# Optimization experiments

Hardware: AMD Instinct MI355X
Metric: run time of the kernel (lower is better)

Reference implementation:

```python
import jax, jax.numpy as jnp
import numpy as np

B, D, H, M = 32, 1024, 1024, 2048
HEBBIAN_LR = 0.05
SCALE = 0.5
TEMP = 1.5
SPARSITY = 0.1
EPS_LN = 1e-6


def _l2_normalize(v, axis=-1):
    # matches tf.nn.l2_normalize: x * rsqrt(max(sum(x^2), 1e-12))
    sq = jnp.sum(v * v, axis=axis, keepdims=True)
    return v * jax.lax.rsqrt(jnp.maximum(sq, 1e-12))


def _layer_norm(v, gamma, beta):
    mu = jnp.mean(v, axis=-1, keepdims=True)
    var = jnp.mean((v - mu) ** 2, axis=-1, keepdims=True)
    return (v - mu) * jax.lax.rsqrt(var + EPS_LN) * gamma + beta


def setup_inputs() -> dict:
    key = jax.random.key(0)
    ks = jax.random.split(key, 8)
    s = 0.02
    return {
        "x": jax.random.normal(ks[0], (B, D), jnp.float32),
        "prev_h": jax.random.normal(ks[1], (B, H), jnp.float32) * 0.01,
        "hebbian_trace": jax.random.normal(ks[2], (M, H), jnp.float32) * 0.01,
        "memory_bank": jax.random.normal(ks[3], (M, H), jnp.float32) * s,
        "W_enc": jax.random.normal(ks[4], (D, H), jnp.float32) * s,
        "b_enc": jnp.zeros((H,), jnp.float32),
        "gamma1": jnp.ones((H,), jnp.float32),
        "beta1": jnp.zeros((H,), jnp.float32),
        "W_int": jax.random.normal(ks[5], (3 * H, 3 * H), jnp.float32) * s,
        "b_int": jnp.zeros((3 * H,), jnp.float32),
        "W_out": jax.random.normal(ks[6], (3 * H, H), jnp.float32) * s,
        "b_out": jnp.zeros((H,), jnp.float32),
        "gamma2": jnp.ones((H,), jnp.float32),
        "beta2": jnp.zeros((H,), jnp.float32),
    }


def reference(x, prev_h, hebbian_trace, memory_bank,
              W_enc, b_enc, gamma1, beta1,
              W_int, b_int, W_out, b_out, gamma2, beta2):
    # input encoder + LN
    z_t = jax.nn.relu(x @ W_enc + b_enc)          # [B,H]
    z_t = _layer_norm(z_t, gamma1, beta1)
    # effective memory = bank + scale * hebbian trace
    eff_mem = memory_bank + SCALE * hebbian_trace  # [M,H]
    # cosine-similarity attention over memory slots
    z_n = _l2_normalize(z_t)
    m_n = _l2_normalize(eff_mem)
    sim = z_n @ m_n.T                               # [B,M]
    sparsity_temp = TEMP / (1.0 + SPARSITY * 10.0)  # = 0.75
    attn = jax.nn.softmax(sim / sparsity_temp, axis=-1)
    m_t = attn @ eff_mem                            # [B,H]
    # integrate and output
    combined = jnp.concatenate([z_t, m_t, prev_h], axis=-1)  # [B,3H]
    hidden = jax.nn.relu(combined @ W_int + b_int)
    h_t = jax.nn.relu(hidden @ W_out + b_out)
    h_t = _layer_norm(h_t, gamma2, beta2)
    # Hebbian trace update: batch-mean outer product attn^T z / B
    mean_update = (attn.T @ z_t) / jnp.asarray(attn.shape[0], z_t.dtype)  # [M,H]
    noise = jax.random.normal(jax.random.key(42), mean_update.shape, mean_update.dtype) * 0.001
    decay = 1.0 - HEBBIAN_LR
    new_trace = hebbian_trace * decay + HEBBIAN_LR * (mean_update + noise)
    new_trace = jnp.clip(new_trace, -0.1, 0.1)
    return h_t, new_trace
```

## Files before the change

### kernel.cpp

```cpp
#include <hip/hip_runtime.h>

typedef unsigned short u16;
typedef unsigned int u32;

#define NB 32
#define NH 1024
#define NM 2048
#define NH3 3072

#define O_Z     0
#define O_RZ    32768
#define O_MT    32800
#define O_HID   65568
#define O_BIG   163872
#define O_ATTN  (O_BIG)
#define O_ATTNP (O_BIG + 65536)
#define O_SQP   (O_BIG + 1114112)
#define O_MTP2  (O_BIG + 65536)
#define O_LMS   (O_BIG + 1146944)

static __device__ __forceinline__ float bf2f(u16 u) {
  union { u32 i; float f; } v; v.i = ((u32)u) << 16; return v.f;
}
static __device__ __forceinline__ u16 f2bf(float f) {
  union { float f; u32 u; } v; v.f = f;
  u32 r = v.u + 0x7FFFu + ((v.u >> 16) & 1u);
  return (u16)(r >> 16);
}
template <bool F32>
static __device__ __forceinline__ float ldT(const void* p, int i) {
  if (F32) return ((const float*)p)[i];
  return bf2f(((const u16*)p)[i]);
}
template <bool F32>
static __device__ __forceinline__ void ld8(const void* p, long i, float o[8]) {
  if (F32) {
    const float4* q = (const float4*)p;
    float4 a = q[i >> 2], b = q[(i >> 2) + 1];
    o[0] = a.x; o[1] = a.y; o[2] = a.z; o[3] = a.w;
    o[4] = b.x; o[5] = b.y; o[6] = b.z; o[7] = b.w;
  } else {
    uint4 u = ((const uint4*)p)[i >> 3];
    o[0] = bf2f((u16)u.x); o[1] = bf2f((u16)(u.x >> 16));
    o[2] = bf2f((u16)u.y); o[3] = bf2f((u16)(u.y >> 16));
    o[4] = bf2f((u16)u.z); o[5] = bf2f((u16)(u.z >> 16));
    o[6] = bf2f((u16)u.w); o[7] = bf2f((u16)(u.w >> 16));
  }
}
template <bool F32>
static __device__ __forceinline__ void st8(void* p, long i, const float o[8]) {
  if (F32) {
    float4* q = (float4*)p;
    float4 a = {o[0], o[1], o[2], o[3]}, b = {o[4], o[5], o[6], o[7]};
    q[i >> 2] = a; q[(i >> 2) + 1] = b;
  } else {
    uint4 u;
    u.x = (u32)f2bf(o[0]) | ((u32)f2bf(o[1]) << 16);
    u.y = (u32)f2bf(o[2]) | ((u32)f2bf(o[3]) << 16);
    u.z = (u32)f2bf(o[4]) | ((u32)f2bf(o[5]) << 16);
    u.w = (u32)f2bf(o[6]) | ((u32)f2bf(o[7]) << 16);
    ((uint4*)p)[i >> 3] = u;
  }
}
template <bool F32>
static __device__ __forceinline__ void stT(void* p, int i, float v) {
  if (F32) ((float*)p)[i] = v;
  else ((u16*)p)[i] = f2bf(v);
}

template <bool F32>
static __device__ __forceinline__ void gemm_core(
    const void* W, int ldw, int k0, int K0, int j0, const float* cs,
    float* dst, int ldd, int l, int w) {
  const int cg = l >> 4, cl = l & 15;
  float acc[8][8];
#pragma unroll
  for (int r = 0; r < 8; ++r)
#pragma unroll
    for (int c = 0; c < 8; ++c) acc[r][c] = 0.f;
#pragma unroll 2
  for (int kk = cg; kk < K0; kk += 4) {
    float wv[8];
    ld8<F32>(W, (long)(k0 + kk) * ldw + j0 + cl * 8, wv);
    const float4* zr = (const float4*)(cs + kk * 36 + w * 8);
    float4 a0 = zr[0], a1 = zr[1];
    float a[8] = {a0.x, a0.y, a0.z, a0.w, a1.x, a1.y, a1.z, a1.w};
#pragma unroll
    for (int r = 0; r < 8; ++r)
#pragma unroll
      for (int c = 0; c < 8; ++c) acc[r][c] += a[r] * wv[c];
  }
#pragma unroll
  for (int r = 0; r < 8; ++r)
#pragma unroll
    for (int c = 0; c < 8; ++c) {
      acc[r][c] += __shfl_xor(acc[r][c], 16);
      acc[r][c] += __shfl_xor(acc[r][c], 32);
    }
#pragma unroll
  for (int r = 0; r < 8; ++r) {
    if ((r >> 1) == cg) {
      float* d = dst + (long)(w * 8 + r) * ldd + j0 + cl * 8;
      float4 v0 = {acc[r][0], acc[r][1], acc[r][2], acc[r][3]};
      float4 v1 = {acc[r][4], acc[r][5], acc[r][6], acc[r][7]};
      ((float4*)d)[0] = v0;
      ((float4*)d)[1] = v1;
    }
  }
}

template <bool F32>
static __device__ void phases(
    int phase, const void* x, const void* prev_h, const void* trace,
    const void* bank, const void* W_enc, const void* b_enc, const void* g1,
    const void* be1, const void* W_int, const void* b_int, const void* W_out,
    const void* b_out, const void* g2, const void* be2, void* outv, float* ws,
    float* sm) {
  const int t = threadIdx.x;
  const int l = t & 63, w = t >> 6;
  const int bx = blockIdx.x;

  if (phase == 1) {
    int j0 = (bx & 7) * 128, ks = bx >> 3, k0 = ks * 64;
    float* cs = sm;
    for (int i = 0; i < 8; ++i) {
      int idx = t + 256 * i; int kk = idx >> 5, bb = idx & 31;
      cs[kk * 36 + bb] = ldT<F32>(x, bb * NH + k0 + kk);
    }
    __syncthreads();
    gemm_core<F32>(W_enc, NH, k0, 64, j0, cs, ws + O_BIG + ks * 32768, NH, l, w);
  } else if (phase == 2) {
    float* red = sm;
    int b = bx, h = t * 4;
    float vv[4];
    vv[0] = ldT<F32>(b_enc, h);     vv[1] = ldT<F32>(b_enc, h + 1);
    vv[2] = ldT<F32>(b_enc, h + 2); vv[3] = ldT<F32>(b_enc, h + 3);
    for (int p = 0; p < 16; ++p) {
      const float4 pv = *(const float4*)&ws[O_BIG + p * 32768 + b * NH + h];
      vv[0] += pv.x; vv[1] += pv.y; vv[2] += pv.z; vv[3] += pv.w;
    }
    float s = 0.f, sq = 0.f;
#pragma unroll
    for (int i = 0; i < 4; ++i) {
      vv[i] = fmaxf(vv[i], 0.f); s += vv[i]; sq += vv[i] * vv[i];
    }
    red[t] = s; __syncthreads();
    for (int d = 128; d > 0; d >>= 1) { if (t < d) red[t] += red[t + d]; __syncthreads(); }
    s = red[0]; __syncthreads();
    red[t] = sq; __syncthreads();
    for (int d = 128; d > 0; d >>= 1) { if (t < d) red[t] += red[t + d]; __syncthreads(); }
    sq = red[0]; __syncthreads();
    float mu = s * (1.f / NH);
    float inv = rsqrtf(sq * (1.f / NH) - mu * mu + 1e-6f);
    float y[4]; float ss = 0.f;
#pragma unroll
    for (int i = 0; i < 4; ++i) {
      y[i] = (vv[i] - mu) * inv * ldT<F32>(g1, h + i) + ldT<F32>(be1, h + i);
      ss += y[i] * y[i];
    }
    float4 y4 = {y[0], y[1], y[2], y[3]};
    *(float4*)&ws[O_Z + b * NH + h] = y4;
    red[t] = ss; __syncthreads();
    for (int d = 128; d > 0; d >>= 1) { if (t < d) red[t] += red[t + d]; __syncthreads(); }
    if (t == 0) ws[O_RZ + b] = rsqrtf(fmaxf(red[0], 1e-12f));
  } else if (phase == 3) {
    int m0 = (bx & 31) * 64, ks = bx >> 5, k0 = ks * 256;
    float* zs = sm;
    for (int i = 0; i < 32; ++i) {
      int idx = t + 256 * i; int kk = idx >> 5, bb = idx & 31;
      zs[idx] = ws[O_Z + bb * NH + k0 + kk];
    }
    __syncthreads();
    int m = m0 + l;
    float acc[32];
#pragma unroll
    for (int i = 0; i < 32; ++i) acc[i] = 0.f;
    float sq = 0.f;
    long rowb = (long)m * NH + k0 + w * 64;
    const float4* zq = (const float4*)(zs + w * 64 * 32);
#pragma unroll 2
    for (int it = 0; it < 8; ++it) {
      float eb[8], et[8];
      ld8<F32>(bank, rowb + it * 8, eb);
      ld8<F32>(trace, rowb + it * 8, et);
#pragma unroll
      for (int kk = 0; kk < 8; ++kk) {
        float e = eb[kk] + 0.5f * et[kk];
        sq += e * e;
        const float4* z4 = zq + (it * 8 + kk) * 8;
#pragma unroll
        for (int bq = 0; bq < 8; ++bq) {
          float4 zv = z4[bq];
          acc[bq * 4 + 0] += e * zv.x; acc[bq * 4 + 1] += e * zv.y;
          acc[bq * 4 + 2] += e * zv.z; acc[bq * 4 + 3] += e * zv.w;
        }
      }
    }
    int p = ks * 4 + w;
#pragma unroll
    for (int bb = 0; bb < 32; ++bb)
      ws[O_ATTNP + p * 65536 + bb * NM + m] = acc[bb];
    ws[O_SQP + p * NM + m] = sq;
  } else if (phase == 4) {
    float* red = sm;
    int b = bx >> 3, mc = bx & 7;
    int m = mc * 256 + t;
    float dot = 0.f, sq = 0.f;
    for (int p = 0; p < 16; ++p) {
      dot += ws[O_ATTNP + p * 65536 + b * NM + m];
      sq  += ws[O_SQP + p * NM + m];
    }
    float rzb = ws[O_RZ + b] * (4.0f / 3.0f);
    float lg = dot * rzb * rsqrtf(fmaxf(sq, 1e-12f));
    ws[O_ATTN + b * NM + m] = lg;
    red[t] = lg; __syncthreads();
    for (int d = 128; d > 0; d >>= 1) { if (t < d) red[t] = fmaxf(red[t], red[t + d]); __syncthreads(); }
    float mx = red[0]; __syncthreads();
    red[t] = __expf(lg - mx); __syncthreads();
    for (int d = 128; d > 0; d >>= 1) { if (t < d) red[t] += red[t + d]; __syncthreads(); }
    if (t == 0) {
      ws[O_LMS + (b * 8 + mc) * 2] = mx;
      ws[O_LMS + (b * 8 + mc) * 2 + 1] = red[0];
    }
  } else if (phase == 5) {
    int j0 = (bx & 7) * 128, ms = bx >> 3, m0 = ms * 64;
    float* cs = sm;
    float* msh = sm + 2304;
    if (t < 32) {
      float M = -1e30f; float lm[8];
#pragma unroll
      for (int i = 0; i < 8; ++i) { lm[i] = ws[O_LMS + (t * 8 + i) * 2]; M = fmaxf(M, lm[i]); }
      float S = 0.f;
#pragma unroll
      for (int i = 0; i < 8; ++i) S += ws[O_LMS + (t * 8 + i) * 2 + 1] * __expf(lm[i] - M);
      msh[2 * t] = M; msh[2 * t + 1] = 1.f / S;
    }
    __syncthreads();
    for (int i = 0; i < 8; ++i) {
      int idx = t + 256 * i; int kk = idx >> 5, bb = idx & 31;
      float lg = ws[O_ATTN + bb * NM + m0 + kk];
      cs[kk * 36 + bb] = __expf(lg - msh[2 * bb]) * msh[2 * bb + 1];
    }
    __syncthreads();
    const int cg = l >> 4, cl = l & 15;
    float acc[8][8];
#pragma unroll
    for (int r = 0; r < 8; ++r)
#pragma unroll
      for (int c = 0; c < 8; ++c) acc[r][c] = 0.f;
#pragma unroll 2
    for (int kk = cg; kk < 64; kk += 4) {
      float eb[8], et[8];
      long src = (long)(m0 + kk) * NH + j0 + cl * 8;
      ld8<F32>(bank, src, eb);
      ld8<F32>(trace, src, et);
      const float4* ar4 = (const float4*)(cs + kk * 36 + w * 8);
      float4 a0 = ar4[0], a1 = ar4[1];
      float a[8] = {a0.x, a0.y, a0.z, a0.w, a1.x, a1.y, a1.z, a1.w};
      float e[8];
#pragma unroll
      for (int c = 0; c < 8; ++c) e[c] = eb[c] + 0.5f * et[c];
#pragma unroll
      for (int r = 0; r < 8; ++r)
#pragma unroll
        for (int c = 0; c < 8; ++c) acc[r][c] += a[r] * e[c];
    }
#pragma unroll
    for (int r = 0; r < 8; ++r)
#pragma unroll
      for (int c = 0; c < 8; ++c) {
        acc[r][c] += __shfl_xor(acc[r][c], 16);
        acc[r][c] += __shfl_xor(acc[r][c], 32);
      }
#pragma unroll
    for (int r = 0; r < 8; ++r) {
      if ((r >> 1) == cg) {
        float* d = ws + O_MTP2 + ms * 32768 + (long)(w * 8 + r) * NH + j0 + cl * 8;
        float4 v0 = {acc[r][0], acc[r][1], acc[r][2], acc[r][3]};
        float4 v1 = {acc[r][4], acc[r][5], acc[r][6], acc[r][7]};
        ((float4*)d)[0] = v0;
        ((float4*)d)[1] = v1;
      }
    }
  } else if (phase == 11) {
    int idx = bx * 256 + t;
    float v = 0.f;
    for (int p = 0; p < 32; ++p) v += ws[O_MTP2 + p * 32768 + idx];
    ws[O_MT + idx] = v;
  } else if (phase == 6) {
    int m0 = (bx >> 3) * 32, h0 = (bx & 7) * 128;
    float* as = sm;
    float* zs = sm + 1024;
    float* msh = sm + 5120;
    if (t < 32) {
      float M = -1e30f; float lm[8];
#pragma unroll
      for (int i = 0; i < 8; ++i) { lm[i] = ws[O_LMS + (t * 8 + i) * 2]; M = fmaxf(M, lm[i]); }
      float S = 0.f;
#pragma unroll
      for (int i = 0; i < 8; ++i) S += ws[O_LMS + (t * 8 + i) * 2 + 1] * __expf(lm[i] - M);
      msh[2 * t] = M; msh[2 * t + 1] = 1.f / S;
    }
    __syncthreads();
    for (int i = 0; i < 4; ++i) {
      int idx = t + 256 * i; int bb = idx >> 5, mm = idx & 31;
      as[idx] = __expf(ws[O_ATTN + bb * NM + m0 + mm] - msh[2 * bb]) * msh[2 * bb + 1];
    }
    for (int i = 0; i < 16; ++i) {
      int idx = t + 256 * i; int bb = idx >> 7, hh = idx & 127;
      zs[idx] = ws[O_Z + bb * NH + h0 + hh];
    }
    __syncthreads();
    const int cg = l >> 4, cl = l & 15;
    const int mA = m0 + cl * 2;
    const int h = h0 + w * 32 + cg * 8;
    float acc0[8], acc1[8];
#pragma unroll
    for (int c = 0; c < 8; ++c) { acc0[c] = 0.f; acc1[c] = 0.f; }
    for (int bb = 0; bb < 32; ++bb) {
      float2 av = *(const float2*)&as[bb * 32 + cl * 2];
      const float4* zr = (const float4*)&zs[bb * 128 + w * 32 + cg * 8];
      float4 z0 = zr[0], z1 = zr[1];
      acc0[0] += av.x * z0.x; acc0[1] += av.x * z0.y;
      acc0[2] += av.x * z0.z; acc0[3] += av.x * z0.w;
      acc0[4] += av.x * z1.x; acc0[5] += av.x * z1.y;
      acc0[6] += av.x * z1.z; acc0[7] += av.x * z1.w;
      acc1[0] += av.y * z0.x; acc1[1] += av.y * z0.y;
      acc1[2] += av.y * z0.z; acc1[3] += av.y * z0.w;
      acc1[4] += av.y * z1.x; acc1[5] += av.y * z1.y;
      acc1[6] += av.y * z1.z; acc1[7] += av.y * z1.w;
    }
    {
      int m = mA;
      float tv[8], o[8];
      ld8<F32>(trace, (long)m * NH + h, tv);
#pragma unroll
      for (int c = 0; c < 8; ++c) {
        float val = tv[c] * 0.95f + 0.0015625f * acc0[c];
        o[c] = fminf(fmaxf(val, -0.1f), 0.1f);
      }
      st8<F32>(outv, (long)NB * NH + (long)m * NH + h, o);
    }
    {
      int m = mA + 1;
      float tv[8], o[8];
      ld8<F32>(trace, (long)m * NH + h, tv);
#pragma unroll
      for (int c = 0; c < 8; ++c) {
        float val = tv[c] * 0.95f + 0.0015625f * acc1[c];
        o[c] = fminf(fmaxf(val, -0.1f), 0.1f);
      }
      st8<F32>(outv, (long)NB * NH + (long)m * NH + h, o);
    }
  } else if (phase == 7) {
    int jc = bx % 24, ks = bx / 24;
    int j0 = jc * 128, k0 = ks * 256;
    float* cs = sm;
    if (ks < 4) {
      for (int i = 0; i < 32; ++i) {
        int idx = t + 256 * i; int kk = idx >> 5, bb = idx & 31;
        cs[kk * 36 + bb] = ws[O_Z + bb * NH + k0 + kk];
      }
    } else if (ks < 8) {
      for (int i = 0; i < 32; ++i) {
        int idx = t + 256 * i; int kk = idx >> 5, bb = idx & 31;
        cs[kk * 36 + bb] = ws[O_MT + bb * NH + (k0 - 1024) + kk];
      }
    } else {
      for (int i = 0; i < 32; ++i) {
        int idx = t + 256 * i; int kk = idx >> 5, bb = idx & 31;
        cs[kk * 36 + bb] = ldT<F32>(prev_h, bb * NH + (k0 - 2048) + kk);
      }
    }
    __syncthreads();
    gemm_core<F32>(W_int, NH3, k0, 256, j0, cs, ws + O_BIG + ks * 98304, NH3, l, w);
  } else if (phase == 8) {
    int idx4 = bx * 256 + t;
    int j = (idx4 % 768) * 4;
    float v0 = ldT<F32>(b_int, j),     v1 = ldT<F32>(b_int, j + 1);
    float v2 = ldT<F32>(b_int, j + 2), v3 = ldT<F32>(b_int, j + 3);
    const float4* pb = (const float4*)(ws + O_BIG);
    for (int p = 0; p < 12; ++p) {
      float4 pv = pb[p * 24576 + idx4];
      v0 += pv.x; v1 += pv.y; v2 += pv.z; v3 += pv.w;
    }
    float4 o = {fmaxf(v0, 0.f), fmaxf(v1, 0.f), fmaxf(v2, 0.f), fmaxf(v3, 0.f)};
    ((float4*)(ws + O_HID))[idx4] = o;
  } else if (phase == 9) {
    int j0 = (bx & 7) * 128, ks = bx >> 3, k0 = ks * 128;
    float* cs = sm;
    for (int i = 0; i < 16; ++i) {
      int idx = t + 256 * i; int kk = idx >> 5, bb = idx & 31;
      cs[kk * 36 + bb] = ws[O_HID + bb * NH3 + k0 + kk];
    }
    __syncthreads();
    gemm_core<F32>(W_out, NH, k0, 128, j0, cs, ws + O_BIG + ks * 32768, NH, l, w);
  } else if (phase == 10) {
    float* red = sm;
    int b = bx, h = t * 4;
    float vv[4];
    vv[0] = ldT<F32>(b_out, h);     vv[1] = ldT<F32>(b_out, h + 1);
    vv[2] = ldT<F32>(b_out, h + 2); vv[3] = ldT<F32>(b_out, h + 3);
    for (int p = 0; p < 24; ++p) {
      const float4 pv = *(const float4*)&ws[O_BIG + p * 32768 + b * NH + h];
      vv[0] += pv.x; vv[1] += pv.y; vv[2] += pv.z; vv[3] += pv.w;
    }
    float s = 0.f, sq = 0.f;
#pragma unroll
    for (int i = 0; i < 4; ++i) {
      vv[i] = fmaxf(vv[i], 0.f); s += vv[i]; sq += vv[i] * vv[i];
    }
    red[t] = s; __syncthreads();
    for (int d = 128; d > 0; d >>= 1) { if (t < d) red[t] += red[t + d]; __syncthreads(); }
    s = red[0]; __syncthreads();
    red[t] = sq; __syncthreads();
    for (int d = 128; d > 0; d >>= 1) { if (t < d) red[t] += red[t + d]; __syncthreads(); }
    sq = red[0];
    float mu = s * (1.f / NH);
    float inv = rsqrtf(sq * (1.f / NH) - mu * mu + 1e-6f);
#pragma unroll
    for (int i = 0; i < 4; ++i) {
      float y = (vv[i] - mu) * inv * ldT<F32>(g2, h + i) + ldT<F32>(be2, h + i);
      stT<F32>(outv, b * NH + h + i, y);
    }
  }
}

__global__ __launch_bounds__(256, 2) void EngramCell_82935818485852_kernel(
    int phase,
    const void* x, const void* prev_h, const void* trace, const void* bank,
    const void* W_enc, const void* b_enc, const void* g1, const void* be1,
    const void* W_int, const void* b_int, const void* W_out, const void* b_out,
    const void* g2, const void* be2,
    void* outv, float* ws) {
  __shared__ float sm[9216];
  const bool f32m = (((const u32*)g1)[0] == 0x3F800000u);
  if (f32m)
    phases<true>(phase, x, prev_h, trace, bank, W_enc, b_enc, g1, be1,
                 W_int, b_int, W_out, b_out, g2, be2, outv, ws, sm);
  else
    phases<false>(phase, x, prev_h, trace, bank, W_enc, b_enc, g1, be1,
                  W_int, b_int, W_out, b_out, g2, be2, outv, ws, sm);
}

extern "C" void kernel_launch(void* const* d_in, const int* in_sizes, int n_in,
                              void* d_out, int out_size, void* d_ws, size_t ws_size,
                              hipStream_t stream) {
  (void)in_sizes; (void)n_in; (void)out_size; (void)ws_size;
  const void* x      = d_in[0];
  const void* prev_h = d_in[1];
  const void* trace  = d_in[2];
  const void* bank   = d_in[3];
  const void* W_enc  = d_in[4];
  const void* b_enc  = d_in[5];
  const void* g1     = d_in[6];
  const void* be1    = d_in[7];
  const void* W_int  = d_in[8];
  const void* b_int  = d_in[9];
  const void* W_out  = d_in[10];
  const void* b_out  = d_in[11];
  const void* g2     = d_in[12];
  const void* be2    = d_in[13];
  float* ws = (float*)d_ws;

  const int order[11] = {1, 2, 3, 4, 5, 11, 6, 7, 8, 9, 10};
  const int grids[12] = {0, 128, 32, 128, 256, 256, 512, 288, 384, 192, 32, 128};
  for (int i = 0; i < 11; ++i) {
    int ph = order[i];
    EngramCell_82935818485852_kernel<<<grids[ph], 256, 0, stream>>>(
        ph, x, prev_h, trace, bank, W_enc, b_enc, g1, be1,
        W_int, b_int, W_out, b_out, g2, be2, d_out, ws);
  }
}
```

Before: 226.7 us.

## Collapse eleven phase launches into six fused phases without split-K partial buffers

Reorganizes the multi-launch pipeline into six phases. The encoder GEMM is fused with its layer norm per batch row. The similarity GEMM now reduces over K inside a block and computes per-chunk softmax statistics. The m_t computation and the trace update share one launch, and the two dense GEMMs reduce over K in-block, so the split-K partial buffers and their separate reduction kernels are gone. This removes global round trips and launch overhead. The cost is far fewer blocks for the big GEMMs (96 and 32), which risks underusing the GPU's compute units and lengthening the serial K loops.

```diff
diff --git a/kernel.cpp b/kernel.cpp
--- a/kernel.cpp
+++ b/kernel.cpp
@@ -14,10 +14,7 @@
 #define O_HID   65568
 #define O_BIG   163872
 #define O_ATTN  (O_BIG)
-#define O_ATTNP (O_BIG + 65536)
-#define O_SQP   (O_BIG + 1114112)
-#define O_MTP2  (O_BIG + 65536)
-#define O_LMS   (O_BIG + 1146944)
+#define O_LMS2  (O_BIG + 65536)
 
 static __device__ __forceinline__ float bf2f(u16 u) {
   union { u32 i; float f; } v; v.i = ((u32)u) << 16; return v.f;
@@ -31,6 +28,12 @@
 static __device__ __forceinline__ float ldT(const void* p, int i) {
   if (F32) return ((const float*)p)[i];
   return bf2f(((const u16*)p)[i]);
+}
+template <bool F32>
+static __device__ __forceinline__ float2 ld2T(const void* p, long i) {
+  if (F32) return ((const float2*)p)[i >> 1];
+  u32 u = ((const u32*)p)[i >> 1];
+  float2 r; r.x = bf2f((u16)u); r.y = bf2f((u16)(u >> 16)); return r;
 }
 template <bool F32>
 static __device__ __forceinline__ void ld8(const void* p, long i, float o[8]) {
@@ -69,48 +72,7 @@
 }
 
 template <bool F32>
-static __device__ __forceinline__ void gemm_core(
-    const void* W, int ldw, int k0, int K0, int j0, const float* cs,
-    float* dst, int ldd, int l, int w) {
-  const int cg = l >> 4, cl = l & 15;
-  float acc[8][8];
-#pragma unroll
-  for (int r = 0; r < 8; ++r)
-#pragma unroll
-    for (int c = 0; c < 8; ++c) acc[r][c] = 0.f;
-#pragma unroll 2
-  for (int kk = cg; kk < K0; kk += 4) {
-    float wv[8];
-    ld8<F32>(W, (long)(k0 + kk) * ldw + j0 + cl * 8, wv);
-    const float4* zr = (const float4*)(cs + kk * 36 + w * 8);
-    float4 a0 = zr[0], a1 = zr[1];
-    float a[8] = {a0.x, a0.y, a0.z, a0.w, a1.x, a1.y, a1.z, a1.w};
-#pragma unroll
-    for (int r = 0; r < 8; ++r)
-#pragma unroll
-      for (int c = 0; c < 8; ++c) acc[r][c] += a[r] * wv[c];
-  }
-#pragma unroll
-  for (int r = 0; r < 8; ++r)
-#pragma unroll
-    for (int c = 0; c < 8; ++c) {
-      acc[r][c] += __shfl_xor(acc[r][c], 16);
-      acc[r][c] += __shfl_xor(acc[r][c], 32);
-    }
-#pragma unroll
-  for (int r = 0; r < 8; ++r) {
-    if ((r >> 1) == cg) {
-      float* d = dst + (long)(w * 8 + r) * ldd + j0 + cl * 8;
-      float4 v0 = {acc[r][0], acc[r][1], acc[r][2], acc[r][3]};
-      float4 v1 = {acc[r][4], acc[r][5], acc[r][6], acc[r][7]};
-      ((float4*)d)[0] = v0;
-      ((float4*)d)[1] = v1;
-    }
-  }
-}
-
-template <bool F32>
-static __device__ void phases(
+static __device__ void run_phase(
     int phase, const void* x, const void* prev_h, const void* trace,
     const void* bank, const void* W_enc, const void* b_enc, const void* g1,
     const void* be1, const void* W_int, const void* b_int, const void* W_out,
@@ -121,73 +83,91 @@
   const int bx = blockIdx.x;
 
   if (phase == 1) {
-    int j0 = (bx & 7) * 128, ks = bx >> 3, k0 = ks * 64;
-    float* cs = sm;
-    for (int i = 0; i < 8; ++i) {
-      int idx = t + 256 * i; int kk = idx >> 5, bb = idx & 31;
-      cs[kk * 36 + bb] = ldT<F32>(x, bb * NH + k0 + kk);
-    }
-    __syncthreads();
-    gemm_core<F32>(W_enc, NH, k0, 64, j0, cs, ws + O_BIG + ks * 32768, NH, l, w);
-  } else if (phase == 2) {
-    float* red = sm;
-    int b = bx, h = t * 4;
-    float vv[4];
-    vv[0] = ldT<F32>(b_enc, h);     vv[1] = ldT<F32>(b_enc, h + 1);
-    vv[2] = ldT<F32>(b_enc, h + 2); vv[3] = ldT<F32>(b_enc, h + 3);
-    for (int p = 0; p < 16; ++p) {
-      const float4 pv = *(const float4*)&ws[O_BIG + p * 32768 + b * NH + h];
-      vv[0] += pv.x; vv[1] += pv.y; vv[2] += pv.z; vv[3] += pv.w;
-    }
-    float s = 0.f, sq = 0.f;
-#pragma unroll
-    for (int i = 0; i < 4; ++i) {
-      vv[i] = fmaxf(vv[i], 0.f); s += vv[i]; sq += vv[i] * vv[i];
+    int b = bx;
+    {
+      float2 v = ld2T<F32>(x, (long)b * NH + 2 * t);
+      sm[2 * t] = v.x; sm[2 * t + 1] = v.y;
+    }
+    __syncthreads();
+    const int tj = t & 127, ts = t >> 7;
+    const int j0 = tj * 8;
+    float acc[8];
+#pragma unroll
+    for (int i = 0; i < 8; ++i) acc[i] = 0.f;
+#pragma unroll 2
+    for (int kk = 0; kk < 256; ++kk) {
+      int k = ts * 256 + kk;
+      float wv[8];
+      ld8<F32>(W_enc, (long)k * NH + j0, wv);
+      float xv = sm[k];
+#pragma unroll
+      for (int i = 0; i < 8; ++i) acc[i] += xv * wv[i];
+    }
+    float* rd = sm + 1024;
+    {
+      float4 a = {acc[0], acc[1], acc[2], acc[3]};
+      float4 c = {acc[4], acc[5], acc[6], acc[7]};
+      *(float4*)&rd[(ts * 128 + tj) * 8] = a;
+      *(float4*)&rd[(ts * 128 + tj) * 8 + 4] = c;
+    }
+    __syncthreads();
+    float* red = sm + 5120;
+    float vv[2]; float s = 0.f, sq = 0.f;
+#pragma unroll
+    for (int jj = 0; jj < 2; ++jj) {
+      int j = t * 2 + jj;
+      float v = ldT<F32>(b_enc, j);
+#pragma unroll
+      for (int q = 0; q < 4; ++q) v += rd[(q * 128 + (j >> 3)) * 8 + (j & 7)];
+      v = fmaxf(v, 0.f);
+      vv[jj] = v; s += v; sq += v * v;
     }
     red[t] = s; __syncthreads();
-    for (int d = 128; d > 0; d >>= 1) { if (t < d) red[t] += red[t + d]; __syncthreads(); }
+    for (int d = 256; d > 0; d >>= 1) { if (t < d) red[t] += red[t + d]; __syncthreads(); }
     s = red[0]; __syncthreads();
     red[t] = sq; __syncthreads();
-    for (int d = 128; d > 0; d >>= 1) { if (t < d) red[t] += red[t + d]; __syncthreads(); }
+    for (int d = 256; d > 0; d >>= 1) { if (t < d) red[t] += red[t + d]; __syncthreads(); }
     sq = red[0]; __syncthreads();
     float mu = s * (1.f / NH);
     float inv = rsqrtf(sq * (1.f / NH) - mu * mu + 1e-6f);
-    float y[4]; float ss = 0.f;
-#pragma unroll
-    for (int i = 0; i < 4; ++i) {
-      y[i] = (vv[i] - mu) * inv * ldT<F32>(g1, h + i) + ldT<F32>(be1, h + i);
-      ss += y[i] * y[i];
-    }
-    float4 y4 = {y[0], y[1], y[2], y[3]};
-    *(float4*)&ws[O_Z + b * NH + h] = y4;
+    float y[2]; float ss = 0.f;
+#pragma unroll
+    for (int jj = 0; jj < 2; ++jj) {
+      int j = t * 2 + jj;
+      y[jj] = (vv[jj] - mu) * inv * ldT<F32>(g1, j) + ldT<F32>(be1, j);
+      ss += y[jj] * y[jj];
+    }
+    float2 y2 = {y[0], y[1]};
+    *(float2*)&ws[O_Z + b * NH + t * 2] = y2;
     red[t] = ss; __syncthreads();
-    for (int d = 128; d > 0; d >>= 1) { if (t < d) red[t] += red[t + d]; __syncthreads(); }
+    for (int d = 256; d > 0; d >>= 1) { if (t < d) red[t] += red[t + d]; __syncthreads(); }
     if (t == 0) ws[O_RZ + b] = rsqrtf(fmaxf(red[0], 1e-12f));
-  } else if (phase == 3) {
-    int m0 = (bx & 31) * 64, ks = bx >> 5, k0 = ks * 256;
+
+  } else if (phase == 2) {
+    const int m0 = bx * 32;
+    const int m = m0 + (l & 31);
+    const int s = w * 2 + (l >> 5);
     float* zs = sm;
-    for (int i = 0; i < 32; ++i) {
-      int idx = t + 256 * i; int kk = idx >> 5, bb = idx & 31;
-      zs[idx] = ws[O_Z + bb * NH + k0 + kk];
-    }
-    __syncthreads();
-    int m = m0 + l;
     float acc[32];
 #pragma unroll
     for (int i = 0; i < 32; ++i) acc[i] = 0.f;
-    float sq = 0.f;
-    long rowb = (long)m * NH + k0 + w * 64;
-    const float4* zq = (const float4*)(zs + w * 64 * 32);
-#pragma unroll 2
-    for (int it = 0; it < 8; ++it) {
-      float eb[8], et[8];
-      ld8<F32>(bank, rowb + it * 8, eb);
-      ld8<F32>(trace, rowb + it * 8, et);
-#pragma unroll
-      for (int kk = 0; kk < 8; ++kk) {
-        float e = eb[kk] + 0.5f * et[kk];
-        sq += e * e;
-        const float4* z4 = zq + (it * 8 + kk) * 8;
+    float sqe = 0.f;
+    for (int c = 0; c < 4; ++c) {
+      __syncthreads();
+      for (int i = 0; i < 16; ++i) {
+        int idx = t + 512 * i; int kk = idx >> 5, bb = idx & 31;
+        zs[idx] = ws[O_Z + bb * NH + c * 256 + kk];
+      }
+      __syncthreads();
+      float eb[8], et[8], eb2[8], et2[8];
+      long rowb = (long)m * NH + c * 256 + s * 16;
+      ld8<F32>(bank, rowb, eb);  ld8<F32>(trace, rowb, et);
+      ld8<F32>(bank, rowb + 8, eb2); ld8<F32>(trace, rowb + 8, et2);
+#pragma unroll
+      for (int q = 0; q < 8; ++q) {
+        float e = eb[q] + 0.5f * et[q];
+        sqe += e * e;
+        const float4* z4 = (const float4*)(zs + (s * 16 + q) * 32);
 #pragma unroll
         for (int bq = 0; bq < 8; ++bq) {
           float4 zv = z4[bq];
@@ -195,216 +175,287 @@
           acc[bq * 4 + 2] += e * zv.z; acc[bq * 4 + 3] += e * zv.w;
         }
       }
-    }
-    int p = ks * 4 + w;
-#pragma unroll
-    for (int bb = 0; bb < 32; ++bb)
-      ws[O_ATTNP + p * 65536 + bb * NM + m] = acc[bb];
-    ws[O_SQP + p * NM + m] = sq;
-  } else if (phase == 4) {
-    float* red = sm;
-    int b = bx >> 3, mc = bx & 7;
-    int m = mc * 256 + t;
-    float dot = 0.f, sq = 0.f;
-    for (int p = 0; p < 16; ++p) {
-      dot += ws[O_ATTNP + p * 65536 + b * NM + m];
-      sq  += ws[O_SQP + p * NM + m];
-    }
-    float rzb = ws[O_RZ + b] * (4.0f / 3.0f);
-    float lg = dot * rzb * rsqrtf(fmaxf(sq, 1e-12f));
-    ws[O_ATTN + b * NM + m] = lg;
-    red[t] = lg; __syncthreads();
-    for (int d = 128; d > 0; d >>= 1) { if (t < d) red[t] = fmaxf(red[t], red[t + d]); __syncthreads(); }
-    float mx = red[0]; __syncthreads();
-    red[t] = __expf(lg - mx); __syncthreads();
-    for (int d = 128; d > 0; d >>= 1) { if (t < d) red[t] += red[t + d]; __syncthreads(); }
-    if (t == 0) {
-      ws[O_LMS + (b * 8 + mc) * 2] = mx;
-      ws[O_LMS + (b * 8 + mc) * 2 + 1] = red[0];
-    }
-  } else if (phase == 5) {
-    int j0 = (bx & 7) * 128, ms = bx >> 3, m0 = ms * 64;
+#pragma unroll
+      for (int q = 0; q < 8; ++q) {
+        float e = eb2[q] + 0.5f * et2[q];
+        sqe += e * e;
+        const float4* z4 = (const float4*)(zs + (s * 16 + 8 + q) * 32);
+#pragma unroll
+        for (int bq = 0; bq < 8; ++bq) {
+          float4 zv = z4[bq];
+          acc[bq * 4 + 0] += e * zv.x; acc[bq * 4 + 1] += e * zv.y;
+          acc[bq * 4 + 2] += e * zv.z; acc[bq * 4 + 3] += e * zv.w;
+        }
+      }
+    }
+#pragma unroll
+    for (int i = 0; i < 32; ++i) acc[i] += __shfl_xor(acc[i], 32);
+    sqe += __shfl_xor(sqe, 32);
+    __syncthreads();
+    float* ps = sm;
+    float* sqp = sm + 8448;
+    float* sq_m = sm + 8704;
+    float* lt = sm + 8736;
+    if (l < 32) {
+#pragma unroll
+      for (int b2 = 0; b2 < 32; ++b2) ps[(w * 32 + l) * 33 + b2] = acc[b2];
+      sqp[w * 32 + l] = sqe;
+    }
+    __syncthreads();
+    if (t < 32) {
+      float v = 0.f;
+#pragma unroll
+      for (int q = 0; q < 8; ++q) v += sqp[q * 32 + t];
+      sq_m[t] = v;
+    }
+    __syncthreads();
+#pragma unroll
+    for (int i = 0; i < 2; ++i) {
+      int q = t * 2 + i; int mm = q >> 5, bb = q & 31;
+      float dot = 0.f;
+#pragma unroll
+      for (int s2 = 0; s2 < 8; ++s2) dot += ps[(s2 * 32 + mm) * 33 + bb];
+      float lg = dot * (ws[O_RZ + bb] * (4.0f / 3.0f)) *
+                 rsqrtf(fmaxf(sq_m[mm], 1e-12f));
+      ws[O_ATTN + bb * NM + m0 + mm] = lg;
+      lt[mm * 33 + bb] = lg;
+    }
+    __syncthreads();
+    if (t < 32) {
+      float mx = -1e30f;
+      for (int mm = 0; mm < 32; ++mm) mx = fmaxf(mx, lt[mm * 33 + t]);
+      float ssum = 0.f;
+      for (int mm = 0; mm < 32; ++mm) ssum += __expf(lt[mm * 33 + t] - mx);
+      ws[O_LMS2 + (t * 64 + bx) * 2] = mx;
+      ws[O_LMS2 + (t * 64 + bx) * 2 + 1] = ssum;
+    }
+
+  } else if (phase == 3) {
+    float* msh = sm;
+    if (t < 32) {
+      float M = -1e30f;
+      for (int ch = 0; ch < 64; ++ch)
+        M = fmaxf(M, ws[O_LMS2 + (t * 64 + ch) * 2]);
+      float S = 0.f;
+      for (int ch = 0; ch < 64; ++ch)
+        S += ws[O_LMS2 + (t * 64 + ch) * 2 + 1] *
+             __expf(ws[O_LMS2 + (t * 64 + ch) * 2] - M);
+      msh[2 * t] = M; msh[2 * t + 1] = 1.f / S;
+    }
+    __syncthreads();
+    if (bx < 32) {
+      float* as_ = sm + 64;
+      float* es = sm + 4672;
+      const int o = w & 3, half = w >> 2;
+      const int cg = l >> 4, cl = l & 15;
+      const int sl = half * 4 + cg;
+      const int h0 = bx * 32;
+      float acc[8][2];
+#pragma unroll
+      for (int r = 0; r < 8; ++r) { acc[r][0] = 0.f; acc[r][1] = 0.f; }
+      for (int c = 0; c < 16; ++c) {
+        __syncthreads();
+        for (int i = 0; i < 8; ++i) {
+          int idx = t * 8 + i; int mm = idx & 127, bb = idx >> 7;
+          float lg = ws[O_ATTN + bb * NM + c * 128 + mm];
+          as_[mm * 36 + bb] = __expf(lg - msh[2 * bb]) * msh[2 * bb + 1];
+        }
+        {
+          int mm = t >> 2, ho = t & 3;
+          float ebv[8], etv[8];
+          long src = (long)(c * 128 + mm) * NH + h0 + ho * 8;
+          ld8<F32>(bank, src, ebv); ld8<F32>(trace, src, etv);
+#pragma unroll
+          for (int i2 = 0; i2 < 8; ++i2)
+            es[mm * 33 + ho * 8 + i2] = ebv[i2] + 0.5f * etv[i2];
+        }
+        __syncthreads();
+#pragma unroll 2
+        for (int kk2 = 0; kk2 < 16; ++kk2) {
+          int mm = sl * 16 + kk2;
+          const float4* a4 = (const float4*)(as_ + mm * 36 + o * 8);
+          float4 a0 = a4[0], a1 = a4[1];
+          float aa[8] = {a0.x, a0.y, a0.z, a0.w, a1.x, a1.y, a1.z, a1.w};
+          float e0 = es[mm * 33 + cl * 2], e1 = es[mm * 33 + cl * 2 + 1];
+#pragma unroll
+          for (int r = 0; r < 8; ++r) {
+            acc[r][0] += aa[r] * e0; acc[r][1] += aa[r] * e1;
+          }
+        }
+      }
+#pragma unroll
+      for (int r = 0; r < 8; ++r)
+#pragma unroll
+        for (int jj = 0; jj < 2; ++jj) {
+          acc[r][jj] += __shfl_xor(acc[r][jj], 16);
+          acc[r][jj] += __shfl_xor(acc[r][jj], 32);
+        }
+      __syncthreads();
+      float* red = sm + 64;
+      if (half == 0 && l < 16) {
+#pragma unroll
+        for (int r = 0; r < 8; ++r) {
+          red[(o * 16 + cl) * 17 + r * 2] = acc[r][0];
+          red[(o * 16 + cl) * 17 + r * 2 + 1] = acc[r][1];
+        }
+      }
+      __syncthreads();
+      if (half == 1 && l < 16) {
+#pragma unroll
+        for (int r = 0; r < 8; ++r) {
+          int b = o * 8 + r;
+          float2 v2;
+          v2.x = acc[r][0] + red[(o * 16 + cl) * 17 + r * 2];
+          v2.y = acc[r][1] + red[(o * 16 + cl) * 17 + r * 2 + 1];
+          *(float2*)&ws[O_MT + b * NH + h0 + cl * 2] = v2;
+        }
+      }
+    } else {
+      const int q = bx - 32;
+      const int u0 = q * 2;
+      const int m0 = (u0 >> 3) * 32;
+      float* as_ = sm + 64;
+      float* zs = sm + 1088;
+      const int half = t >> 8, t2 = t & 255;
+      const int l2 = t2 & 63, w2 = t2 >> 6;
+      const int cg2 = l2 >> 4, cl2 = l2 & 15;
+      const int h0h = ((u0 + half) & 7) * 128;
+#pragma unroll
+      for (int i = 0; i < 2; ++i) {
+        int idx = t * 2 + i; int bb = idx >> 5, mm = idx & 31;
+        as_[idx] = __expf(ws[O_ATTN + bb * NM + m0 + mm] - msh[2 * bb]) *
+                   msh[2 * bb + 1];
+      }
+      for (int i = 0; i < 16; ++i) {
+        int idx = t2 + 256 * i; int bb = idx >> 7, hh = idx & 127;
+        zs[half * 4096 + idx] = ws[O_Z + bb * NH + h0h + hh];
+      }
+      __syncthreads();
+      const float* zsh = zs + half * 4096;
+      const int mA = m0 + cl2 * 2;
+      const int h = h0h + w2 * 32 + cg2 * 8;
+      float acc0[8], acc1[8];
+#pragma unroll
+      for (int c = 0; c < 8; ++c) { acc0[c] = 0.f; acc1[c] = 0.f; }
+      for (int bb = 0; bb < NB; ++bb) {
+        float2 av = *(const float2*)&as_[bb * 32 + cl2 * 2];
+        const float4* zr = (const float4*)&zsh[bb * 128 + w2 * 32 + cg2 * 8];
+        float4 z0 = zr[0], z1 = zr[1];
+        acc0[0] += av.x * z0.x; acc0[1] += av.x * z0.y;
+        acc0[2] += av.x * z0.z; acc0[3] += av.x * z0.w;
+        acc0[4] += av.x * z1.x; acc0[5] += av.x * z1.y;
+        acc0[6] += av.x * z1.z; acc0[7] += av.x * z1.w;
+        acc1[0] += av.y * z0.x; acc1[1] += av.y * z0.y;
+        acc1[2] += av.y * z0.z; acc1[3] += av.y * z0.w;
+        acc1[4] += av.y * z1.x; acc1[5] += av.y * z1.y;
+        acc1[6] += av.y * z1.z; acc1[7] += av.y * z1.w;
+      }
+      {
+        int mm = mA;
+        float tv[8], o8[8];
+        ld8<F32>(trace, (long)mm * NH + h, tv);
+#pragma unroll
+        for (int c = 0; c < 8; ++c) {
+          float val = tv[c] * 0.95f + 0.0015625f * acc0[c];
+          o8[c] = fminf(fmaxf(val, -0.1f), 0.1f);
+        }
+        st8<F32>(outv, (long)NB * NH + (long)mm * NH + h, o8);
+      }
+      {
+        int mm = mA + 1;
+        float tv[8], o8[8];
+        ld8<F32>(trace, (long)mm * NH + h, tv);
+#pragma unroll
+        for (int c = 0; c < 8; ++c) {
+          float val = tv[c] * 0.95f + 0.0015625f * acc1[c];
+          o8[c] = fminf(fmaxf(val, -0.1f), 0.1f);
+        }
+        st8<F32>(outv, (long)NB * NH + (long)mm * NH + h, o8);
+      }
+    }
+
+  } else if (phase == 4 || phase == 5) {
+    const void* Wp = (phase == 4) ? W_int : W_out;
+    const int ldw = (phase == 4) ? NH3 : NH;
+    const int j0 = bx * 32;
     float* cs = sm;
-    float* msh = sm + 2304;
-    if (t < 32) {
-      float M = -1e30f; float lm[8];
-#pragma unroll
-      for (int i = 0; i < 8; ++i) { lm[i] = ws[O_LMS + (t * 8 + i) * 2]; M = fmaxf(M, lm[i]); }
-      float S = 0.f;
-#pragma unroll
-      for (int i = 0; i < 8; ++i) S += ws[O_LMS + (t * 8 + i) * 2 + 1] * __expf(lm[i] - M);
-      msh[2 * t] = M; msh[2 * t + 1] = 1.f / S;
-    }
-    __syncthreads();
-    for (int i = 0; i < 8; ++i) {
-      int idx = t + 256 * i; int kk = idx >> 5, bb = idx & 31;
-      float lg = ws[O_ATTN + bb * NM + m0 + kk];
-      cs[kk * 36 + bb] = __expf(lg - msh[2 * bb]) * msh[2 * bb + 1];
-    }
-    __syncthreads();
+    float* red = sm + 9216;
+    const int o = w & 3, half = w >> 2;
     const int cg = l >> 4, cl = l & 15;
-    float acc[8][8];
+    const int sl = half * 4 + cg;
+    float acc[8][2];
+#pragma unroll
+    for (int r = 0; r < 8; ++r) { acc[r][0] = 0.f; acc[r][1] = 0.f; }
+    for (int c = 0; c < 12; ++c) {
+      __syncthreads();
+      for (int i = 0; i < 16; ++i) {
+        int idx = t + 512 * i; int kk = idx >> 5, bb = idx & 31;
+        int k = c * 256 + kk;
+        float v;
+        if (phase == 5) v = ws[O_HID + bb * NH3 + k];
+        else if (k < 1024) v = ws[O_Z + bb * NH + k];
+        else if (k < 2048) v = ws[O_MT + bb * NH + k - 1024];
+        else v = ldT<F32>(prev_h, bb * NH + k - 2048);
+        cs[kk * 36 + bb] = v;
+      }
+      __syncthreads();
+#pragma unroll 2
+      for (int kk2 = 0; kk2 < 32; ++kk2) {
+        int kk = sl * 32 + kk2;
+        float2 wv = ld2T<F32>(Wp, (long)(c * 256 + kk) * ldw + j0 + cl * 2);
+        const float4* a4 = (const float4*)(cs + kk * 36 + o * 8);
+        float4 a0 = a4[0], a1 = a4[1];
+        float aa[8] = {a0.x, a0.y, a0.z, a0.w, a1.x, a1.y, a1.z, a1.w};
+#pragma unroll
+        for (int r = 0; r < 8; ++r) {
+          acc[r][0] += aa[r] * wv.x; acc[r][1] += aa[r] * wv.y;
+        }
+      }
+    }
 #pragma unroll
     for (int r = 0; r < 8; ++r)
 #pragma unroll
-      for (int c = 0; c < 8; ++c) acc[r][c] = 0.f;
-#pragma unroll 2
-    for (int kk = cg; kk < 64; kk += 4) {
-      float eb[8], et[8];
-      long src = (long)(m0 + kk) * NH + j0 + cl * 8;
-      ld8<F32>(bank, src, eb);
-      ld8<F32>(trace, src, et);
-      const float4* ar4 = (const float4*)(cs + kk * 36 + w * 8);
-      float4 a0 = ar4[0], a1 = ar4[1];
-      float a[8] = {a0.x, a0.y, a0.z, a0.w, a1.x, a1.y, a1.z, a1.w};
-      float e[8];
-#pragma unroll
-      for (int c = 0; c < 8; ++c) e[c] = eb[c] + 0.5f * et[c];
-#pragma unroll
-      for (int r = 0; r < 8; ++r)
-#pragma unroll
-        for (int c = 0; c < 8; ++c) acc[r][c] += a[r] * e[c];
-    }
-#pragma unroll
-    for (int r = 0; r < 8; ++r)
-#pragma unroll
-      for (int c = 0; c < 8; ++c) {
-        acc[r][c] += __shfl_xor(acc[r][c], 16);
-        acc[r][c] += __shfl_xor(acc[r][c], 32);
-      }
-#pragma unroll
-    for (int r = 0; r < 8; ++r) {
-      if ((r >> 1) == cg) {
-        float* d = ws + O_MTP2 + ms * 32768 + (long)(w * 8 + r) * NH + j0 + cl * 8;
-        float4 v0 = {acc[r][0], acc[r][1], acc[r][2], acc[r][3]};
-        float4 v1 = {acc[r][4], acc[r][5], acc[r][6], acc[r][7]};
-        ((float4*)d)[0] = v0;
-        ((float4*)d)[1] = v1;
-      }
-    }
-  } else if (phase == 11) {
-    int idx = bx * 256 + t;
-    float v = 0.f;
-    for (int p = 0; p < 32; ++p) v += ws[O_MTP2 + p * 32768 + idx];
-    ws[O_MT + idx] = v;
+      for (int jj = 0; jj < 2; ++jj) {
+        acc[r][jj] += __shfl_xor(acc[r][jj], 16);
+        acc[r][jj] += __shfl_xor(acc[r][jj], 32);
+      }
+    __syncthreads();
+    if (half == 0 && l < 16) {
+#pragma unroll
+      for (int r = 0; r < 8; ++r) {
+        red[(o * 16 + cl) * 17 + r * 2] = acc[r][0];
+        red[(o * 16 + cl) * 17 + r * 2 + 1] = acc[r][1];
+      }
+    }
+    __syncthreads();
+    if (half == 1 && l < 16) {
+#pragma unroll
+      for (int r = 0; r < 8; ++r) {
+        int b = o * 8 + r;
+        float v0 = acc[r][0] + red[(o * 16 + cl) * 17 + r * 2];
+        float v1 = acc[r][1] + red[(o * 16 + cl) * 17 + r * 2 + 1];
+        if (phase == 4) {
+          int j = j0 + cl * 2;
+          v0 = fmaxf(v0 + ldT<F32>(b_int, j), 0.f);
+          v1 = fmaxf(v1 + ldT<F32>(b_int, j + 1), 0.f);
+          float2 v2 = {v0, v1};
+          *(float2*)&ws[O_HID + b * NH3 + j] = v2;
+        } else {
+          float2 v2 = {v0, v1};
+          *(float2*)&ws[O_BIG + b * NH + j0 + cl * 2] = v2;
+        }
+      }
+    }
+
   } else if (phase == 6) {
-    int m0 = (bx >> 3) * 32, h0 = (bx & 7) * 128;
-    float* as = sm;
-    float* zs = sm + 1024;
-    float* msh = sm + 5120;
-    if (t < 32) {
-      float M = -1e30f; float lm[8];
-#pragma unroll
-      for (int i = 0; i < 8; ++i) { lm[i] = ws[O_LMS + (t * 8 + i) * 2]; M = fmaxf(M, lm[i]); }
-      float S = 0.f;
-#pragma unroll
-      for (int i = 0; i < 8; ++i) S += ws[O_LMS + (t * 8 + i) * 2 + 1] * __expf(lm[i] - M);
-      msh[2 * t] = M; msh[2 * t + 1] = 1.f / S;
-    }
-    __syncthreads();
-    for (int i = 0; i < 4; ++i) {
-      int idx = t + 256 * i; int bb = idx >> 5, mm = idx & 31;
-      as[idx] = __expf(ws[O_ATTN + bb * NM + m0 + mm] - msh[2 * bb]) * msh[2 * bb + 1];
-    }
-    for (int i = 0; i < 16; ++i) {
-      int idx = t + 256 * i; int bb = idx >> 7, hh = idx & 127;
-      zs[idx] = ws[O_Z + bb * NH + h0 + hh];
-    }
-    __syncthreads();
-    const int cg = l >> 4, cl = l & 15;
-    const int mA = m0 + cl * 2;
-    const int h = h0 + w * 32 + cg * 8;
-    float acc0[8], acc1[8];
-#pragma unroll
-    for (int c = 0; c < 8; ++c) { acc0[c] = 0.f; acc1[c] = 0.f; }
-    for (int bb = 0; bb < 32; ++bb) {
-      float2 av = *(const float2*)&as[bb * 32 + cl * 2];
-      const float4* zr = (const float4*)&zs[bb * 128 + w * 32 + cg * 8];
-      float4 z0 = zr[0], z1 = zr[1];
-      acc0[0] += av.x * z0.x; acc0[1] += av.x * z0.y;
-      acc0[2] += av.x * z0.z; acc0[3] += av.x * z0.w;
-      acc0[4] += av.x * z1.x; acc0[5] += av.x * z1.y;
-      acc0[6] += av.x * z1.z; acc0[7] += av.x * z1.w;
-      acc1[0] += av.y * z0.x; acc1[1] += av.y * z0.y;
-      acc1[2] += av.y * z0.z; acc1[3] += av.y * z0.w;
-      acc1[4] += av.y * z1.x; acc1[5] += av.y * z1.y;
-      acc1[6] += av.y * z1.z; acc1[7] += av.y * z1.w;
-    }
-    {
-      int m = mA;
-      float tv[8], o[8];
-      ld8<F32>(trace, (long)m * NH + h, tv);
-#pragma unroll
-      for (int c = 0; c < 8; ++c) {
-        float val = tv[c] * 0.95f + 0.0015625f * acc0[c];
-        o[c] = fminf(fmaxf(val, -0.1f), 0.1f);
-      }
-      st8<F32>(outv, (long)NB * NH + (long)m * NH + h, o);
-    }
-    {
-      int m = mA + 1;
-      float tv[8], o[8];
-      ld8<F32>(trace, (long)m * NH + h, tv);
-#pragma unroll
-      for (int c = 0; c < 8; ++c) {
-        float val = tv[c] * 0.95f + 0.0015625f * acc1[c];
-        o[c] = fminf(fmaxf(val, -0.1f), 0.1f);
-      }
-      st8<F32>(outv, (long)NB * NH + (long)m * NH + h, o);
-    }
-  } else if (phase == 7) {
-    int jc = bx % 24, ks = bx / 24;
-    int j0 = jc * 128, k0 = ks * 256;
-    float* cs = sm;
-    if (ks < 4) {
-      for (int i = 0; i < 32; ++i) {
-        int idx = t + 256 * i; int kk = idx >> 5, bb = idx & 31;
-        cs[kk * 36 + bb] = ws[O_Z + bb * NH + k0 + kk];
-      }
-    } else if (ks < 8) {
-      for (int i = 0; i < 32; ++i) {
-        int idx = t + 256 * i; int kk = idx >> 5, bb = idx & 31;
-        cs[kk * 36 + bb] = ws[O_MT + bb * NH + (k0 - 1024) + kk];
-      }
-    } else {
-      for (int i = 0; i < 32; ++i) {
-        int idx = t + 256 * i; int kk = idx >> 5, bb = idx & 31;
-        cs[kk * 36 + bb] = ldT<F32>(prev_h, bb * NH + (k0 - 2048) + kk);
-      }
-    }
-    __syncthreads();
-    gemm_core<F32>(W_int, NH3, k0, 256, j0, cs, ws + O_BIG + ks * 98304, NH3, l, w);
-  } else if (phase == 8) {
-    int idx4 = bx * 256 + t;
-    int j = (idx4 % 768) * 4;
-    float v0 = ldT<F32>(b_int, j),     v1 = ldT<F32>(b_int, j + 1);
-    float v2 = ldT<F32>(b_int, j + 2), v3 = ldT<F32>(b_int, j + 3);
-    const float4* pb = (const float4*)(ws + O_BIG);
-    for (int p = 0; p < 12; ++p) {
-      float4 pv = pb[p * 24576 + idx4];
-      v0 += pv.x; v1 += pv.y; v2 += pv.z; v3 += pv.w;
-    }
-    float4 o = {fmaxf(v0, 0.f), fmaxf(v1, 0.f), fmaxf(v2, 0.f), fmaxf(v3, 0.f)};
-    ((float4*)(ws + O_HID))[idx4] = o;
-  } else if (phase == 9) {
-    int j0 = (bx & 7) * 128, ks = bx >> 3, k0 = ks * 128;
-    float* cs = sm;
-    for (int i = 0; i < 16; ++i) {
-      int idx = t + 256 * i; int kk = idx >> 5, bb = idx & 31;
-      cs[kk * 36 + bb] = ws[O_HID + bb * NH3 + k0 + kk];
-    }
-    __syncthreads();
-    gemm_core<F32>(W_out, NH, k0, 128, j0, cs, ws + O_BIG + ks * 32768, NH, l, w);
-  } else if (phase == 10) {
     float* red = sm;
     int b = bx, h = t * 4;
+    float4 pv = *(const float4*)&ws[O_BIG + b * NH + h];
     float vv[4];
-    vv[0] = ldT<F32>(b_out, h);     vv[1] = ldT<F32>(b_out, h + 1);
-    vv[2] = ldT<F32>(b_out, h + 2); vv[3] = ldT<F32>(b_out, h + 3);
-    for (int p = 0; p < 24; ++p) {
-      const float4 pv = *(const float4*)&ws[O_BIG + p * 32768 + b * NH + h];
-      vv[0] += pv.x; vv[1] += pv.y; vv[2] += pv.z; vv[3] += pv.w;
-    }
+    vv[0] = ldT<F32>(b_out, h) + pv.x;
+    vv[1] = ldT<F32>(b_out, h + 1) + pv.y;
+    vv[2] = ldT<F32>(b_out, h + 2) + pv.z;
+    vv[3] = ldT<F32>(b_out, h + 3) + pv.w;
     float s = 0.f, sq = 0.f;
 #pragma unroll
     for (int i = 0; i < 4; ++i) {
@@ -426,21 +477,21 @@
   }
 }
 
-__global__ __launch_bounds__(256, 2) void EngramCell_82935818485852_kernel(
+__global__ __launch_bounds__(512) void EngramCell_82935818485852_kernel(
     int phase,
     const void* x, const void* prev_h, const void* trace, const void* bank,
     const void* W_enc, const void* b_enc, const void* g1, const void* be1,
     const void* W_int, const void* b_int, const void* W_out, const void* b_out,
     const void* g2, const void* be2,
     void* outv, float* ws) {
-  __shared__ float sm[9216];
+  extern __shared__ float sm[];
   const bool f32m = (((const u32*)g1)[0] == 0x3F800000u);
   if (f32m)
-    phases<true>(phase, x, prev_h, trace, bank, W_enc, b_enc, g1, be1,
-                 W_int, b_int, W_out, b_out, g2, be2, outv, ws, sm);
+    run_phase<true>(phase, x, prev_h, trace, bank, W_enc, b_enc, g1, be1,
+                    W_int, b_int, W_out, b_out, g2, be2, outv, ws, sm);
   else
-    phases<false>(phase, x, prev_h, trace, bank, W_enc, b_enc, g1, be1,
-                  W_int, b_int, W_out, b_out, g2, be2, outv, ws, sm);
+    run_phase<false>(phase, x, prev_h, trace, bank, W_enc, b_enc, g1, be1,
+                     W_int, b_int, W_out, b_out, g2, be2, outv, ws, sm);
 }
 
 extern "C" void kernel_launch(void* const* d_in, const int* in_sizes, int n_in,
@@ -463,11 +514,13 @@
   const void* be2    = d_in[13];
   float* ws = (float*)d_ws;
 
-  const int order[11] = {1, 2, 3, 4, 5, 11, 6, 7, 8, 9, 10};
-  const int grids[12] = {0, 128, 32, 128, 256, 256, 512, 288, 384, 192, 32, 128};
-  for (int i = 0; i < 11; ++i) {
-    int ph = order[i];
-    EngramCell_82935818485852_kernel<<<grids[ph], 256, 0, stream>>>(
+  const int grids[7]   = {0, 32, 64, 288, 96, 32, 32};
+  const int threads[7] = {0, 512, 512, 512, 512, 512, 256};
+  const int shmem[7]   = {0, 5632 * 4, 9792 * 4, 9280 * 4, 10304 * 4,
+                          10304 * 4, 256 * 4};
+  for (int ph = 1; ph <= 6; ++ph) {
+    EngramCell_82935818485852_kernel<<<grids[ph], threads[ph], shmem[ph],
+                                       stream>>>(
         ph, x, prev_h, trace, bank, W_enc, b_enc, g1, be1,
         W_int, b_int, W_out, b_out, g2, be2, d_out, ws);
   }
```

Result: slower. 531.1 us (+134.3%).
